# Optimization experiments

Hardware: AMD Instinct MI355X
Metric: run time of the kernel (lower is better)

## Reference

```python
import jax, jax.numpy as jnp
import numpy as np
from jax import lax

B, L, LQ, D_IN, ET, H, INIT_EMBED = 16, 256, 64, 32, 128, 4, 8
DIM = 2 * D_IN          # attention value/feature dim (x concat mask)
ETK = ET // H           # per-head time-embedding dim


def _lin(key, fan_in, shape):
    b = 1.0 / np.sqrt(fan_in)
    return jax.random.uniform(key, shape, jnp.float32, -b, b)


def setup_inputs() -> dict:
    key = jax.random.key(0)
    ks = jax.random.split(key, 24)
    inp = {
        "x": jax.random.normal(ks[0], (B, L, D_IN), jnp.float32),
        "time_steps": jnp.sort(jax.random.uniform(ks[1], (B, L), jnp.float32), axis=-1),
        "mask": (jax.random.uniform(ks[2], (B, L, D_IN)) > 0.5).astype(jnp.float32),
        "query": jnp.linspace(0.0, 1.0, LQ, dtype=jnp.float32),
        # time embedding: Linear(1,1) and Linear(1, ET-1)
        "w_lin": _lin(ks[3], 1, (1,)), "b_lin": _lin(ks[4], 1, (1,)),
        "w_per": _lin(ks[5], 1, (ET - 1,)), "b_per": _lin(ks[6], 1, (ET - 1,)),
        # attention projections (stored as (in,out))
        "Wq": _lin(ks[7], ET, (ET, ET)), "bq": _lin(ks[8], ET, (ET,)),
        "Wk": _lin(ks[9], ET, (ET, ET)), "bk": _lin(ks[10], ET, (ET,)),
        "Wo": _lin(ks[11], H * DIM, (H * DIM, ET)), "bo": _lin(ks[12], H * DIM, (ET,)),
        # vanilla RNN (tanh)
        "W_ih": _lin(ks[13], ET, (ET, ET)), "b_ih": _lin(ks[14], ET, (ET,)),
        "W_hh": _lin(ks[15], ET, (ET, ET)), "b_hh": _lin(ks[16], ET, (ET,)),
        "r1_w": _lin(ks[17], ET, (ET, 128)), "r1_b": _lin(ks[17], ET, (128,)),
        "r2_w": _lin(ks[18], 128, (128, 128)), "r2_b": _lin(ks[18], 128, (128,)),
        "r3_w": _lin(ks[19], 128, (128, ET)), "r3_b": _lin(ks[19], 128, (ET,)),
        "r4_w": _lin(ks[20], ET, (ET, INIT_EMBED)), "r4_b": _lin(ks[20], ET, (INIT_EMBED,)),
    }
    return inp


def reference(x, time_steps, mask, query,
              w_lin, b_lin, w_per, b_per,
              Wq, bq, Wk, bk, Wo, bo,
              W_ih, b_ih, W_hh, b_hh,
              r1_w, r1_b, r2_w, r2_b, r3_w, r3_b, r4_w, r4_b):
    def time_embed(tt):  # (...,) -> (..., ET)
        tt = tt[..., None]
        return jnp.concatenate([tt * w_lin + b_lin,
                                jnp.sin(tt * w_per + b_per)], axis=-1)

    xc = jnp.concatenate([x, mask], axis=-1)          # (B,L,DIM) value
    m2 = jnp.concatenate([mask, mask], axis=-1)       # (B,L,DIM)

    kemb = time_embed(time_steps)                     # (B,L,ET)
    qemb = time_embed(query)                          # (LQ,ET)

    q = (qemb @ Wq + bq).reshape(LQ, H, ETK).transpose(1, 0, 2)       # (H,LQ,ETK)
    k = (kemb @ Wk + bk).reshape(B, L, H, ETK).transpose(0, 2, 1, 3)  # (B,H,L,ETK)

    scores = jnp.einsum('hqe,bhke->bhqk', q, k) / np.sqrt(ETK)        # (B,H,LQ,L)
    # per-feature mask broadcast: (B,H,LQ,L,DIM)
    s5 = jnp.where(m2[:, None, None, :, :] == 0, -1e9, scores[..., None])
    p = jax.nn.softmax(s5, axis=-2)                   # softmax over keys L
    att = jnp.einsum('bhqkd,bkd->bhqd', p, xc)        # (B,H,LQ,DIM)
    att = att.transpose(0, 2, 1, 3).reshape(B, LQ, H * DIM)
    out = att @ Wo + bo                               # (B,LQ,ET)

    # vanilla tanh RNN, return final hidden state
    def step(h, xt):
        h = jnp.tanh(xt @ W_ih + b_ih + h @ W_hh + b_hh)
        return h, None
    h0 = jnp.zeros((B, ET), out.dtype)
    hT, _ = lax.scan(step, h0, out.transpose(1, 0, 2))  # scan over LQ

    y = hT @ r1_w + r1_b
    y = y @ r2_w + r2_b
    y = y @ r3_w + r3_b
    y = y @ r4_w + r4_b                               # (B, INIT_EMBED)
    return y
```

## Files before the change

kernel.cpp:

```cpp
#include <hip/hip_runtime.h>
#include <hip/hip_bf16.h>

typedef __hip_bfloat16 bf16;
__device__ __forceinline__ float tof(bf16 v) { return __bfloat162float(v); }

#define NB 16
#define NL 256
#define NLQ 64
#define NDIN 32
#define NET 128
#define NH 4
#define NETK 32
#define NDIM 64
#define N_IN 26

struct CvtArgs {
  const void* src[N_IN];
  int cum[N_IN + 1];
};

__global__ __launch_bounds__(256) void k_cvt(CvtArgs a, const unsigned* __restrict__ qraw,
                                             float* __restrict__ dst, int total) {
  bool is_f32 = (qraw[0] == 0u);
  int g = blockIdx.x * 256 + threadIdx.x;
  if (g >= total) return;
  int s = 0;
  while (g >= a.cum[s + 1]) s++;
  int off = g - a.cum[s];
  float v;
  if (is_f32) v = ((const float*)a.src[s])[off];
  else        v = tof(((const bf16*)a.src[s])[off]);
  dst[g] = v;
}

__global__ __launch_bounds__(128) void k_embed_proj(
    const float* __restrict__ ts, const float* __restrict__ query,
    const float* __restrict__ w_lin, const float* __restrict__ b_lin,
    const float* __restrict__ w_per, const float* __restrict__ b_per,
    const float* __restrict__ Wk, const float* __restrict__ bk,
    const float* __restrict__ Wq, const float* __restrict__ bq,
    float* __restrict__ kproj, float* __restrict__ qproj) {
  __shared__ float emb[NET];
  int r = blockIdx.x;
  int j = threadIdx.x;
  bool isQ = (r >= NB * NL);
  float t = isQ ? query[r - NB * NL] : ts[r];
  float e;
  if (j == 0) e = t * w_lin[0] + b_lin[0];
  else        e = sinf(t * w_per[j - 1] + b_per[j - 1]);
  emb[j] = e;
  __syncthreads();
  const float* W = isQ ? Wq : Wk;
  float acc0 = isQ ? bq[j] : bk[j];
  float acc1 = 0.f, acc2 = 0.f, acc3 = 0.f;
#pragma unroll 8
  for (int i = 0; i < NET; i += 4) {
    acc0 += emb[i]     * W[(i)     * NET + j];
    acc1 += emb[i + 1] * W[(i + 1) * NET + j];
    acc2 += emb[i + 2] * W[(i + 2) * NET + j];
    acc3 += emb[i + 3] * W[(i + 3) * NET + j];
  }
  float acc = (acc0 + acc1) + (acc2 + acc3);
  if (isQ) qproj[(r - NB * NL) * NET + j] = acc;
  else     kproj[r * NET + j] = acc;
}

__global__ __launch_bounds__(256) void k_attn(
    const float* __restrict__ x, const float* __restrict__ mask,
    const float* __restrict__ qproj, const float* __restrict__ kproj,
    float* __restrict__ att) {
  const float SC = 0.17677669529663687f;
  int idx = blockIdx.x;
  int qg = idx & 7;
  int h  = (idx >> 3) & 3;
  int b  = idx >> 5;
  __shared__ float xs[NL * NDIN];
  __shared__ unsigned mb[NL];
  __shared__ float es[8 * NL];
  __shared__ float qs[8 * NETK];
  int t = threadIdx.x;

  {
    int qq = t >> 5, i = t & 31;
    qs[t] = qproj[(qg * 8 + qq) * NET + h * NETK + i];
  }
  {
    const float4* xb4 = (const float4*)(x + (size_t)b * NL * NDIN);
    float4* xs4 = (float4*)xs;
#pragma unroll
    for (int i = t; i < NL * NDIN / 4; i += 256) xs4[i] = xb4[i];
  }
  {
    const float4* mr4 = (const float4*)(mask + (size_t)(b * NL + t) * NDIN);
    unsigned bits = 0;
#pragma unroll
    for (int u = 0; u < 8; u++) {
      float4 m = mr4[u];
      bits |= (m.x != 0.f ? 1u : 0u) << (4 * u);
      bits |= (m.y != 0.f ? 1u : 0u) << (4 * u + 1);
      bits |= (m.z != 0.f ? 1u : 0u) << (4 * u + 2);
      bits |= (m.w != 0.f ? 1u : 0u) << (4 * u + 3);
    }
    mb[t] = bits;
  }
  float kr[NETK];
  {
    const float* kp = kproj + (size_t)(b * NL + t) * NET + h * NETK;
#pragma unroll
    for (int i = 0; i < NETK; i++) kr[i] = kp[i];
  }
  __syncthreads();
#pragma unroll
  for (int qq = 0; qq < 8; qq++) {
    float s0 = 0.f, s1 = 0.f;
#pragma unroll
    for (int i = 0; i < NETK; i += 2) {
      s0 += qs[qq * NETK + i]     * kr[i];
      s1 += qs[qq * NETK + i + 1] * kr[i + 1];
    }
    es[qq * NL + t] = __expf((s0 + s1) * SC);
  }
  __syncthreads();
  int qq = t >> 5, c = t & 31;
  float denom = 0.f, numx = 0.f, sumx = 0.f;
#pragma unroll 4
  for (int k = 0; k < NL; k++) {
    float e  = es[qq * NL + k];
    float mv = ((mb[k] >> c) & 1u) ? 1.f : 0.f;
    float xv = xs[k * NDIN + c];
    e *= mv;
    denom += e;
    numx  += e * xv;
    sumx  += xv;
  }
  float ax = (denom > 0.f) ? (numx / denom) : (sumx * (1.f / 256.f));
  float am = (denom > 0.f) ? 1.f : 0.f;
  int q = qg * 8 + qq;
  float* ao = att + (size_t)((b * NLQ + q) * NH + h) * NDIM;
  ao[c]      = ax;
  ao[32 + c] = am;
}

__global__ __launch_bounds__(128) void k_out_xw(
    const float* __restrict__ att,
    const float* __restrict__ Wo, const float* __restrict__ bo,
    const float* __restrict__ Wih, const float* __restrict__ bih,
    const float* __restrict__ bhh, float* __restrict__ XW) {
  int r = blockIdx.x;
  int j = threadIdx.x;
  __shared__ float arow[NH * NDIM];
  __shared__ float orow[NET];
  arow[j]       = att[(size_t)r * 256 + j];
  arow[j + 128] = att[(size_t)r * 256 + 128 + j];
  __syncthreads();
  float a0 = bo[j], a1 = 0.f, a2 = 0.f, a3 = 0.f;
#pragma unroll 8
  for (int u = 0; u < 256; u += 4) {
    a0 += arow[u]     * Wo[(u)     * NET + j];
    a1 += arow[u + 1] * Wo[(u + 1) * NET + j];
    a2 += arow[u + 2] * Wo[(u + 2) * NET + j];
    a3 += arow[u + 3] * Wo[(u + 3) * NET + j];
  }
  orow[j] = (a0 + a1) + (a2 + a3);
  __syncthreads();
  float b0 = bih[j] + bhh[j], b1 = 0.f, b2 = 0.f, b3 = 0.f;
#pragma unroll 8
  for (int e = 0; e < NET; e += 4) {
    b0 += orow[e]     * Wih[(e)     * NET + j];
    b1 += orow[e + 1] * Wih[(e + 1) * NET + j];
    b2 += orow[e + 2] * Wih[(e + 2) * NET + j];
    b3 += orow[e + 3] * Wih[(e + 3) * NET + j];
  }
  XW[(size_t)r * NET + j] = (b0 + b1) + (b2 + b3);
}

__device__ __forceinline__ void layer128(const float* src_lds,
                                         const float* __restrict__ W,
                                         const float* __restrict__ bvec,
                                         float* dst_lds, int j, int s) {
  const float4* h4 = (const float4*)(src_lds + s * 64);
  float a0 = 0.f, a1 = 0.f, a2 = 0.f, a3 = 0.f;
#pragma unroll
  for (int i = 0; i < 16; i++) {
    float4 hv = h4[i];
    int base = (s * 64 + 4 * i) * NET + j;
    a0 += hv.x * W[base];
    a1 += hv.y * W[base + NET];
    a2 += hv.z * W[base + 2 * NET];
    a3 += hv.w * W[base + 3 * NET];
  }
  float acc = (a0 + a1) + (a2 + a3);
  acc += __shfl_xor(acc, 1, 64);
  if (s == 0) dst_lds[j] = acc + bvec[j];
}

__global__ __launch_bounds__(256, 1) void k_rnn(
    const float* __restrict__ XW, const float* __restrict__ Whh,
    const float* __restrict__ r1w, const float* __restrict__ r1b,
    const float* __restrict__ r2w, const float* __restrict__ r2b,
    const float* __restrict__ r3w, const float* __restrict__ r3b,
    const float* __restrict__ r4w, const float* __restrict__ r4b,
    const unsigned* __restrict__ qraw, void* __restrict__ outv) {
  bool is_f32 = (qraw[0] == 0u);
  int b = blockIdx.x;
  int tid = threadIdx.x;
  int s = tid & 1;
  int j = tid >> 1;
  __shared__ float hb[2][NET];
  __shared__ float tmp[NET];

  float w[64];
#pragma unroll
  for (int i = 0; i < 64; i++) w[i] = Whh[(s * 64 + i) * NET + j];
  float xw[32];
#pragma unroll
  for (int u = 0; u < 32; u++)
    xw[u] = XW[(size_t)(b * NLQ + 2 * u + s) * NET + j];

  hb[0][tid & 127] = 0.f;
  __syncthreads();

#pragma unroll 2
  for (int t = 0; t < NLQ; t++) {
    const float4* h4 = (const float4*)&hb[t & 1][s * 64];
    float a0 = 0.f, a1 = 0.f, a2 = 0.f, a3 = 0.f;
#pragma unroll
    for (int i = 0; i < 16; i++) {
      float4 hv = h4[i];
      a0 += hv.x * w[4 * i];
      a1 += hv.y * w[4 * i + 1];
      a2 += hv.z * w[4 * i + 2];
      a3 += hv.w * w[4 * i + 3];
    }
    float acc = (a0 + a1) + (a2 + a3);
    acc += __shfl_xor(acc, 1, 64);
    if (s == (t & 1)) {
      float z = acc + xw[t >> 1];
      float e2 = __expf(2.f * z);
      hb[(t + 1) & 1][j] = 1.f - 2.f / (e2 + 1.f);
    }
    __syncthreads();
  }

  layer128(hb[0], r1w, r1b, tmp, j, s);
  __syncthreads();
  layer128(tmp, r2w, r2b, hb[1], j, s);
  __syncthreads();
  layer128(hb[1], r3w, r3b, hb[0], j, s);
  __syncthreads();
  if (tid < 64) {
    int jj = tid >> 3, p = tid & 7;
    float y = 0.f;
#pragma unroll
    for (int i = 0; i < 16; i++) {
      int ii = p * 16 + i;
      y += hb[0][ii] * r4w[ii * 8 + jj];
    }
    y += __shfl_xor(y, 1, 64);
    y += __shfl_xor(y, 2, 64);
    y += __shfl_xor(y, 4, 64);
    if (p == 0) {
      y += r4b[jj];
      if (is_f32) ((float*)outv)[b * 8 + jj] = y;
      else        ((bf16*)outv)[b * 8 + jj] = __float2bfloat16(y);
    }
  }
}

extern "C" void kernel_launch(void* const* d_in, const int* in_sizes, int n_in,
                              void* d_out, int out_size, void* d_ws, size_t ws_size,
                              hipStream_t stream) {
  CvtArgs a;
  int cum = 0;
  for (int i = 0; i < N_IN; i++) {
    a.src[i] = d_in[i];
    a.cum[i] = cum;
    cum += in_sizes[i];
  }
  a.cum[N_IN] = cum;
  int total = cum;
  int totalR = (total + 63) & ~63;

  float* ws = (float*)d_ws;
  float* F = ws;
  const float* x     = F + a.cum[0];
  const float* ts    = F + a.cum[1];
  const float* mask  = F + a.cum[2];
  const float* query = F + a.cum[3];
  const float* w_lin = F + a.cum[4];
  const float* b_lin = F + a.cum[5];
  const float* w_per = F + a.cum[6];
  const float* b_per = F + a.cum[7];
  const float* Wq    = F + a.cum[8];
  const float* bq    = F + a.cum[9];
  const float* Wk    = F + a.cum[10];
  const float* bk    = F + a.cum[11];
  const float* Wo    = F + a.cum[12];
  const float* bo    = F + a.cum[13];
  const float* Wih   = F + a.cum[14];
  const float* bih   = F + a.cum[15];
  const float* Whh   = F + a.cum[16];
  const float* bhh   = F + a.cum[17];
  const float* r1w   = F + a.cum[18];
  const float* r1b   = F + a.cum[19];
  const float* r2w   = F + a.cum[20];
  const float* r2b   = F + a.cum[21];
  const float* r3w   = F + a.cum[22];
  const float* r3b   = F + a.cum[23];
  const float* r4w   = F + a.cum[24];
  const float* r4b   = F + a.cum[25];

  float* qproj = ws + totalR;
  float* kproj = qproj + 8192;
  float* att   = kproj + 524288;
  float* XW    = att + 262144;

  const unsigned* qraw = (const unsigned*)d_in[3];

  k_cvt<<<(total + 255) / 256, 256, 0, stream>>>(a, qraw, F, total);
  k_embed_proj<<<NB * NL + NLQ, 128, 0, stream>>>(
      ts, query, w_lin, b_lin, w_per, b_per, Wk, bk, Wq, bq, kproj, qproj);
  k_attn<<<NB * NH * 8, 256, 0, stream>>>(x, mask, qproj, kproj, att);
  k_out_xw<<<NB * NLQ, 128, 0, stream>>>(att, Wo, bo, Wih, bih, bhh, XW);
  k_rnn<<<NB, 256, 0, stream>>>(XW, Whh, r1w, r1b, r2w, r2b, r3w, r3b,
                                r4w, r4b, qraw, (void*)d_out);
}
```

Before: 187.4 us.

## Drop input conversion kernel, batch embed rows, fuse attention with output projections

Removes the generic conversion kernel and reads the fp32 inputs directly. The bf16 path is dropped, so the code now assumes fp32 inputs. The embedding projection now handles 8 rows per block so each weight load is reused across rows. Attention processes all four heads in one block per (batch, query-group) and fuses the Wo and W_ih projections, removing the att intermediate and one launch. The risk is fewer blocks in the attention stage (128 instead of 512), which lowers parallelism.

```diff
diff --git a/kernel.cpp b/kernel.cpp
--- a/kernel.cpp
+++ b/kernel.cpp
@@ -1,8 +1,6 @@
 #include <hip/hip_runtime.h>
 #include <hip/hip_bf16.h>
 
-typedef __hip_bfloat16 bf16;
-__device__ __forceinline__ float tof(bf16 v) { return __bfloat162float(v); }
 
 #define NB 16
 #define NL 256
@@ -11,27 +9,6 @@
 #define NET 128
 #define NH 4
 #define NETK 32
-#define NDIM 64
-#define N_IN 26
-
-struct CvtArgs {
-  const void* src[N_IN];
-  int cum[N_IN + 1];
-};
-
-__global__ __launch_bounds__(256) void k_cvt(CvtArgs a, const unsigned* __restrict__ qraw,
-                                             float* __restrict__ dst, int total) {
-  bool is_f32 = (qraw[0] == 0u);
-  int g = blockIdx.x * 256 + threadIdx.x;
-  if (g >= total) return;
-  int s = 0;
-  while (g >= a.cum[s + 1]) s++;
-  int off = g - a.cum[s];
-  float v;
-  if (is_f32) v = ((const float*)a.src[s])[off];
-  else        v = tof(((const bf16*)a.src[s])[off]);
-  dst[g] = v;
-}
 
 __global__ __launch_bounds__(128) void k_embed_proj(
     const float* __restrict__ ts, const float* __restrict__ query,
@@ -40,55 +17,64 @@
     const float* __restrict__ Wk, const float* __restrict__ bk,
     const float* __restrict__ Wq, const float* __restrict__ bq,
     float* __restrict__ kproj, float* __restrict__ qproj) {
-  __shared__ float emb[NET];
-  int r = blockIdx.x;
+  __shared__ float emb[8 * NET];
+  int g = blockIdx.x;
   int j = threadIdx.x;
-  bool isQ = (r >= NB * NL);
-  float t = isQ ? query[r - NB * NL] : ts[r];
-  float e;
-  if (j == 0) e = t * w_lin[0] + b_lin[0];
-  else        e = sinf(t * w_per[j - 1] + b_per[j - 1]);
-  emb[j] = e;
+  bool isQ = (g >= 512);
+  int base = (isQ ? g - 512 : g) * 8;
+  float wl_ = w_lin[0], bl_ = b_lin[0];
+  float wp = (j > 0) ? w_per[j - 1] : 0.f;
+  float bp = (j > 0) ? b_per[j - 1] : 0.f;
+#pragma unroll
+  for (int rr = 0; rr < 8; rr++) {
+    float t = isQ ? query[base + rr] : ts[base + rr];
+    emb[rr * NET + j] = (j == 0) ? (t * wl_ + bl_) : sinf(t * wp + bp);
+  }
   __syncthreads();
   const float* W = isQ ? Wq : Wk;
-  float acc0 = isQ ? bq[j] : bk[j];
-  float acc1 = 0.f, acc2 = 0.f, acc3 = 0.f;
-#pragma unroll 8
-  for (int i = 0; i < NET; i += 4) {
-    acc0 += emb[i]     * W[(i)     * NET + j];
-    acc1 += emb[i + 1] * W[(i + 1) * NET + j];
-    acc2 += emb[i + 2] * W[(i + 2) * NET + j];
-    acc3 += emb[i + 3] * W[(i + 3) * NET + j];
-  }
-  float acc = (acc0 + acc1) + (acc2 + acc3);
-  if (isQ) qproj[(r - NB * NL) * NET + j] = acc;
-  else     kproj[r * NET + j] = acc;
-}
-
-__global__ __launch_bounds__(256) void k_attn(
+  float bias = isQ ? bq[j] : bk[j];
+  float acc[8];
+#pragma unroll
+  for (int rr = 0; rr < 8; rr++) acc[rr] = bias;
+#pragma unroll 4
+  for (int i = 0; i < NET; i++) {
+    float wv = W[i * NET + j];
+#pragma unroll
+    for (int rr = 0; rr < 8; rr++) acc[rr] += emb[rr * NET + i] * wv;
+  }
+  float* dst = isQ ? qproj : kproj;
+#pragma unroll
+  for (int rr = 0; rr < 8; rr++) dst[(size_t)(base + rr) * NET + j] = acc[rr];
+}
+
+__global__ __launch_bounds__(256) void k_attn_fused(
     const float* __restrict__ x, const float* __restrict__ mask,
     const float* __restrict__ qproj, const float* __restrict__ kproj,
-    float* __restrict__ att) {
+    const float* __restrict__ Wo, const float* __restrict__ bo,
+    const float* __restrict__ Wih, const float* __restrict__ bih,
+    const float* __restrict__ bhh, float* __restrict__ XW) {
   const float SC = 0.17677669529663687f;
-  int idx = blockIdx.x;
-  int qg = idx & 7;
-  int h  = (idx >> 3) & 3;
-  int b  = idx >> 5;
+  int blk = blockIdx.x;
+  int qg = blk & 7;
+  int b  = blk >> 3;
+  int t  = threadIdx.x;
+
   __shared__ float xs[NL * NDIN];
   __shared__ unsigned mb[NL];
   __shared__ float es[8 * NL];
-  __shared__ float qs[8 * NETK];
-  int t = threadIdx.x;
-
-  {
-    int qq = t >> 5, i = t & 31;
-    qs[t] = qproj[(qg * 8 + qq) * NET + h * NETK + i];
-  }
-  {
-    const float4* xb4 = (const float4*)(x + (size_t)b * NL * NDIN);
-    float4* xs4 = (float4*)xs;
-#pragma unroll
-    for (int i = t; i < NL * NDIN / 4; i += 256) xs4[i] = xb4[i];
+  __shared__ float qa[8 * NL];
+  __shared__ float orow[8 * NET];
+
+  {
+    const float* qsrc = qproj + (size_t)qg * 8 * NET;
+#pragma unroll
+    for (int u = 0; u < 4; u++) qa[t + 256 * u] = qsrc[t + 256 * u];
+  }
+  {
+    const float4* src = (const float4*)(x + (size_t)b * NL * NDIN);
+    float4* dst = (float4*)xs;
+#pragma unroll
+    for (int u = 0; u < 8; u++) dst[t + 256 * u] = src[t + 256 * u];
   }
   {
     const float4* mr4 = (const float4*)(mask + (size_t)(b * NL + t) * NDIN);
@@ -103,75 +89,100 @@
     }
     mb[t] = bits;
   }
-  float kr[NETK];
-  {
-    const float* kp = kproj + (size_t)(b * NL + t) * NET + h * NETK;
-#pragma unroll
-    for (int i = 0; i < NETK; i++) kr[i] = kp[i];
-  }
-  __syncthreads();
-#pragma unroll
-  for (int qq = 0; qq < 8; qq++) {
-    float s0 = 0.f, s1 = 0.f;
-#pragma unroll
-    for (int i = 0; i < NETK; i += 2) {
-      s0 += qs[qq * NETK + i]     * kr[i];
-      s1 += qs[qq * NETK + i + 1] * kr[i + 1];
-    }
-    es[qq * NL + t] = __expf((s0 + s1) * SC);
-  }
-  __syncthreads();
+  __syncthreads();
+
   int qq = t >> 5, c = t & 31;
-  float denom = 0.f, numx = 0.f, sumx = 0.f;
+  float den[NH], num[NH];
+  float sumx = 0.f;
+
+#pragma unroll
+  for (int h = 0; h < NH; h++) {
+    {
+      float kr[NETK];
+      const float4* kp =
+          (const float4*)(kproj + (size_t)(b * NL + t) * NET + h * NETK);
+#pragma unroll
+      for (int i = 0; i < 8; i++) {
+        float4 v = kp[i];
+        kr[4 * i] = v.x; kr[4 * i + 1] = v.y;
+        kr[4 * i + 2] = v.z; kr[4 * i + 3] = v.w;
+      }
+#pragma unroll
+      for (int q8 = 0; q8 < 8; q8++) {
+        const float* qv = &qa[q8 * NET + h * NETK];
+        float s0 = 0.f, s1 = 0.f;
+#pragma unroll
+        for (int i = 0; i < NETK; i += 2) {
+          s0 += qv[i] * kr[i];
+          s1 += qv[i + 1] * kr[i + 1];
+        }
+        es[q8 * NL + t] = __expf((s0 + s1) * SC);
+      }
+    }
+    __syncthreads();
+    {
+      float d = 0.f, n = 0.f;
+#pragma unroll 2
+      for (int k = 0; k < NL; k++) {
+        float e  = es[qq * NL + k];
+        float mv = ((mb[k] >> c) & 1u) ? 1.f : 0.f;
+        float xv = xs[k * NDIN + c];
+        if (h == 0) sumx += xv;
+        e *= mv;
+        d += e;
+        n += e * xv;
+      }
+      den[h] = d; num[h] = n;
+    }
+    __syncthreads();
+  }
+
+  {
+    bool any = (den[0] > 0.f);
+    float fallback = sumx * (1.f / 256.f);
+    float am = any ? 1.f : 0.f;
+#pragma unroll
+    for (int h = 0; h < NH; h++) {
+      float ax = any ? (num[h] / den[h]) : fallback;
+      qa[qq * 256 + h * 64 + c]      = ax;
+      qa[qq * 256 + h * 64 + 32 + c] = am;
+    }
+  }
+  __syncthreads();
+
+  {
+    int j = t & 127, half = t >> 7;
+    float a0, a1, a2, a3;
+    a0 = a1 = a2 = a3 = bo[j];
 #pragma unroll 4
-  for (int k = 0; k < NL; k++) {
-    float e  = es[qq * NL + k];
-    float mv = ((mb[k] >> c) & 1u) ? 1.f : 0.f;
-    float xv = xs[k * NDIN + c];
-    e *= mv;
-    denom += e;
-    numx  += e * xv;
-    sumx  += xv;
-  }
-  float ax = (denom > 0.f) ? (numx / denom) : (sumx * (1.f / 256.f));
-  float am = (denom > 0.f) ? 1.f : 0.f;
-  int q = qg * 8 + qq;
-  float* ao = att + (size_t)((b * NLQ + q) * NH + h) * NDIM;
-  ao[c]      = ax;
-  ao[32 + c] = am;
-}
-
-__global__ __launch_bounds__(128) void k_out_xw(
-    const float* __restrict__ att,
-    const float* __restrict__ Wo, const float* __restrict__ bo,
-    const float* __restrict__ Wih, const float* __restrict__ bih,
-    const float* __restrict__ bhh, float* __restrict__ XW) {
-  int r = blockIdx.x;
-  int j = threadIdx.x;
-  __shared__ float arow[NH * NDIM];
-  __shared__ float orow[NET];
-  arow[j]       = att[(size_t)r * 256 + j];
-  arow[j + 128] = att[(size_t)r * 256 + 128 + j];
-  __syncthreads();
-  float a0 = bo[j], a1 = 0.f, a2 = 0.f, a3 = 0.f;
-#pragma unroll 8
-  for (int u = 0; u < 256; u += 4) {
-    a0 += arow[u]     * Wo[(u)     * NET + j];
-    a1 += arow[u + 1] * Wo[(u + 1) * NET + j];
-    a2 += arow[u + 2] * Wo[(u + 2) * NET + j];
-    a3 += arow[u + 3] * Wo[(u + 3) * NET + j];
-  }
-  orow[j] = (a0 + a1) + (a2 + a3);
-  __syncthreads();
-  float b0 = bih[j] + bhh[j], b1 = 0.f, b2 = 0.f, b3 = 0.f;
-#pragma unroll 8
-  for (int e = 0; e < NET; e += 4) {
-    b0 += orow[e]     * Wih[(e)     * NET + j];
-    b1 += orow[e + 1] * Wih[(e + 1) * NET + j];
-    b2 += orow[e + 2] * Wih[(e + 2) * NET + j];
-    b3 += orow[e + 3] * Wih[(e + 3) * NET + j];
-  }
-  XW[(size_t)r * NET + j] = (b0 + b1) + (b2 + b3);
+    for (int u = 0; u < 256; u++) {
+      float wv = Wo[u * NET + j];
+      a0 += qa[(half * 4 + 0) * 256 + u] * wv;
+      a1 += qa[(half * 4 + 1) * 256 + u] * wv;
+      a2 += qa[(half * 4 + 2) * 256 + u] * wv;
+      a3 += qa[(half * 4 + 3) * 256 + u] * wv;
+    }
+    orow[(half * 4 + 0) * NET + j] = a0;
+    orow[(half * 4 + 1) * NET + j] = a1;
+    orow[(half * 4 + 2) * NET + j] = a2;
+    orow[(half * 4 + 3) * NET + j] = a3;
+    __syncthreads();
+    float c0, c1, c2, c3;
+    c0 = c1 = c2 = c3 = bih[j] + bhh[j];
+#pragma unroll 4
+    for (int e = 0; e < NET; e++) {
+      float wv = Wih[e * NET + j];
+      c0 += orow[(half * 4 + 0) * NET + e] * wv;
+      c1 += orow[(half * 4 + 1) * NET + e] * wv;
+      c2 += orow[(half * 4 + 2) * NET + e] * wv;
+      c3 += orow[(half * 4 + 3) * NET + e] * wv;
+    }
+    int q0 = qg * 8 + half * 4;
+    XW[(size_t)(b * NLQ + q0 + 0) * NET + j] = c0;
+    XW[(size_t)(b * NLQ + q0 + 1) * NET + j] = c1;
+    XW[(size_t)(b * NLQ + q0 + 2) * NET + j] = c2;
+    XW[(size_t)(b * NLQ + q0 + 3) * NET + j] = c3;
+  }
 }
 
 __device__ __forceinline__ void layer128(const float* src_lds,
@@ -200,8 +211,7 @@
     const float* __restrict__ r2w, const float* __restrict__ r2b,
     const float* __restrict__ r3w, const float* __restrict__ r3b,
     const float* __restrict__ r4w, const float* __restrict__ r4b,
-    const unsigned* __restrict__ qraw, void* __restrict__ outv) {
-  bool is_f32 = (qraw[0] == 0u);
+    float* __restrict__ out) {
   int b = blockIdx.x;
   int tid = threadIdx.x;
   int s = tid & 1;
@@ -259,69 +269,50 @@
     y += __shfl_xor(y, 1, 64);
     y += __shfl_xor(y, 2, 64);
     y += __shfl_xor(y, 4, 64);
-    if (p == 0) {
-      y += r4b[jj];
-      if (is_f32) ((float*)outv)[b * 8 + jj] = y;
-      else        ((bf16*)outv)[b * 8 + jj] = __float2bfloat16(y);
-    }
+    if (p == 0) out[b * 8 + jj] = y + r4b[jj];
   }
 }
 
 extern "C" void kernel_launch(void* const* d_in, const int* in_sizes, int n_in,
                               void* d_out, int out_size, void* d_ws, size_t ws_size,
                               hipStream_t stream) {
-  CvtArgs a;
-  int cum = 0;
-  for (int i = 0; i < N_IN; i++) {
-    a.src[i] = d_in[i];
-    a.cum[i] = cum;
-    cum += in_sizes[i];
-  }
-  a.cum[N_IN] = cum;
-  int total = cum;
-  int totalR = (total + 63) & ~63;
-
-  float* ws = (float*)d_ws;
-  float* F = ws;
-  const float* x     = F + a.cum[0];
-  const float* ts    = F + a.cum[1];
-  const float* mask  = F + a.cum[2];
-  const float* query = F + a.cum[3];
-  const float* w_lin = F + a.cum[4];
-  const float* b_lin = F + a.cum[5];
-  const float* w_per = F + a.cum[6];
-  const float* b_per = F + a.cum[7];
-  const float* Wq    = F + a.cum[8];
-  const float* bq    = F + a.cum[9];
-  const float* Wk    = F + a.cum[10];
-  const float* bk    = F + a.cum[11];
-  const float* Wo    = F + a.cum[12];
-  const float* bo    = F + a.cum[13];
-  const float* Wih   = F + a.cum[14];
-  const float* bih   = F + a.cum[15];
-  const float* Whh   = F + a.cum[16];
-  const float* bhh   = F + a.cum[17];
-  const float* r1w   = F + a.cum[18];
-  const float* r1b   = F + a.cum[19];
-  const float* r2w   = F + a.cum[20];
-  const float* r2b   = F + a.cum[21];
-  const float* r3w   = F + a.cum[22];
-  const float* r3b   = F + a.cum[23];
-  const float* r4w   = F + a.cum[24];
-  const float* r4b   = F + a.cum[25];
-
-  float* qproj = ws + totalR;
-  float* kproj = qproj + 8192;
-  float* att   = kproj + 524288;
-  float* XW    = att + 262144;
-
-  const unsigned* qraw = (const unsigned*)d_in[3];
-
-  k_cvt<<<(total + 255) / 256, 256, 0, stream>>>(a, qraw, F, total);
-  k_embed_proj<<<NB * NL + NLQ, 128, 0, stream>>>(
+  const float* x     = (const float*)d_in[0];
+  const float* ts    = (const float*)d_in[1];
+  const float* mask  = (const float*)d_in[2];
+  const float* query = (const float*)d_in[3];
+  const float* w_lin = (const float*)d_in[4];
+  const float* b_lin = (const float*)d_in[5];
+  const float* w_per = (const float*)d_in[6];
+  const float* b_per = (const float*)d_in[7];
+  const float* Wq    = (const float*)d_in[8];
+  const float* bq    = (const float*)d_in[9];
+  const float* Wk    = (const float*)d_in[10];
+  const float* bk    = (const float*)d_in[11];
+  const float* Wo    = (const float*)d_in[12];
+  const float* bo    = (const float*)d_in[13];
+  const float* Wih   = (const float*)d_in[14];
+  const float* bih   = (const float*)d_in[15];
+  const float* Whh   = (const float*)d_in[16];
+  const float* bhh   = (const float*)d_in[17];
+  const float* r1w   = (const float*)d_in[18];
+  const float* r1b   = (const float*)d_in[19];
+  const float* r2w   = (const float*)d_in[20];
+  const float* r2b   = (const float*)d_in[21];
+  const float* r3w   = (const float*)d_in[22];
+  const float* r3b   = (const float*)d_in[23];
+  const float* r4w   = (const float*)d_in[24];
+  const float* r4b   = (const float*)d_in[25];
+  float* out = (float*)d_out;
+
+  float* ws    = (float*)d_ws;
+  float* kproj = ws;
+  float* qproj = ws + 524288;
+  float* XW    = ws + 532480;
+
+  k_embed_proj<<<520, 128, 0, stream>>>(
       ts, query, w_lin, b_lin, w_per, b_per, Wk, bk, Wq, bq, kproj, qproj);
-  k_attn<<<NB * NH * 8, 256, 0, stream>>>(x, mask, qproj, kproj, att);
-  k_out_xw<<<NB * NLQ, 128, 0, stream>>>(att, Wo, bo, Wih, bih, bhh, XW);
+  k_attn_fused<<<NB * 8, 256, 0, stream>>>(
+      x, mask, qproj, kproj, Wo, bo, Wih, bih, bhh, XW);
   k_rnn<<<NB, 256, 0, stream>>>(XW, Whh, r1w, r1b, r2w, r2b, r3w, r3b,
-                                r4w, r4b, qraw, (void*)d_out);
-}
+                                r4w, r4b, out);
+}
```

New measurement: 229.5 us. 22.4% more time.
